# Kernel optimization log

Hardware: AMD Instinct MI355X
Metric: run time of the kernel (lower is better)

Reference implementation:

```python
import jax, jax.numpy as jnp
import numpy as np

EPS = 1e-12

def setup_inputs() -> dict:
    key = jax.random.key(0)
    k1, k2, k3, k4, k5, k6 = jax.random.split(key, 6)
    B, DIM, T = 16, 256, 2048
    K, D = 1024, 64  # num_embeddings, embedding_dim
    N = B * T
    input_data = jax.random.normal(k1, (B, DIM, T), dtype=jnp.float32)
    codebooks = jax.random.normal(k2, (K, D), dtype=jnp.float32)
    W_in = jax.random.normal(k3, (DIM, D), dtype=jnp.float32) / np.sqrt(DIM)
    b_in = jnp.zeros((D,), dtype=jnp.float32)
    W_out = jax.random.normal(k4, (D, DIM), dtype=jnp.float32) / np.sqrt(D)
    b_out = jnp.zeros((DIM,), dtype=jnp.float32)
    random_vector = jax.random.normal(k5, (N, D), dtype=jnp.float32)
    return {"input_data": input_data, "codebooks": codebooks,
            "W_in": W_in, "b_in": b_in, "W_out": W_out, "b_out": b_out,
            "random_vector": random_vector}

def reference(input_data, codebooks, W_in, b_in, W_out, b_out, random_vector):
    B, DIM, T = input_data.shape
    D = codebooks.shape[1]
    # encode: [B, DIM, T] -> [B, T, DIM] -> project -> [B*T, D]
    x = jnp.einsum('bct,cd->btd', input_data, W_in) + b_in
    x = x.reshape(-1, D)  # [N, D]
    distances = (jnp.sum(x * x, axis=1, keepdims=True)
                 - 2.0 * (x @ codebooks.T)
                 + jnp.sum(codebooks * codebooks, axis=1)[None, :])  # [N, K]
    min_indices = jnp.argmin(distances, axis=1)  # [N]
    hard = codebooks[min_indices]  # [N, D]
    # noise substitution
    norm_resid = jnp.sqrt(jnp.sum((x - hard) ** 2, axis=1, keepdims=True))
    norm_rand = jnp.sqrt(jnp.sum(random_vector ** 2, axis=1, keepdims=True))
    vq_error = (norm_resid / (norm_rand + EPS)) * random_vector
    q = x + vq_error  # [N, D]
    # decode: [N, D] -> [B, T, D] -> project_out -> [B, DIM, T]
    q = q.reshape(B, T, D)
    out = jnp.einsum('btd,dc->bct', q, W_out) + b_out[None, :, None]
    return out
```

## Files before the change

### kernel.cpp

```cpp
#include <hip/hip_runtime.h>
#include <hip/hip_bf16.h>

typedef __bf16 bf16x8 __attribute__((ext_vector_type(8)));
typedef unsigned short u16x8 __attribute__((ext_vector_type(8)));
typedef unsigned short u16x4 __attribute__((ext_vector_type(4)));
typedef float f32x4 __attribute__((ext_vector_type(4)));
typedef unsigned short u16;

constexpr int DIMc = 256, Tt = 2048, Kk = 1024, Dd = 64;

#define WS_WINT 0
#define WS_CBX  18432
#define WS_WOX  116736

__device__ __forceinline__ u16 f2b(float f) {
  unsigned u = __float_as_uint(f);
  return (u16)((u + 0x7FFFu + ((u >> 16) & 1u)) >> 16);
}
__device__ __forceinline__ float b2f(u16 v) {
  return __uint_as_float(((unsigned)v) << 16);
}
__device__ __forceinline__ f32x4 mfma16(u16x8 a, u16x8 b, f32x4 c) {
  return __builtin_amdgcn_mfma_f32_16x16x32_bf16(
      __builtin_bit_cast(bf16x8, a), __builtin_bit_cast(bf16x8, b), c, 0, 0, 0);
}
__device__ __forceinline__ void dma16(const u16* g, u16* l) {
  __builtin_amdgcn_global_load_lds(
      (const __attribute__((address_space(1))) unsigned int*)g,
      (__attribute__((address_space(3))) unsigned int*)l, 16, 0, 0);
}

__global__ void nsvq_prep(const float* __restrict__ cb, const float* __restrict__ Win,
                          const float* __restrict__ bin, const float* __restrict__ Wout,
                          const float* __restrict__ bout, u16* __restrict__ wsu) {
  const int g = blockIdx.x * 256 + threadIdx.x;
  u16* WinT = wsu + WS_WINT;
  u16* CbX  = wsu + WS_CBX;
  u16* WoX  = wsu + WS_WOX;
  for (int i = g; i < 16384; i += 8192) {
    int c = i >> 6, d = i & 63;
    WinT[d * 288 + c] = f2b(Win[i]);
  }
  if (g < 2048) {
    int d = g >> 5, j = g & 31; u16 v = 0;
    float bv = bin[d]; u16 h = f2b(bv);
    if (j == 0) v = h; else if (j == 1) v = f2b(bv - b2f(h));
    WinT[d * 288 + 256 + j] = v;
  }
  if (g < 1024) {
    const float4* cr = (const float4*)(cb + (size_t)g * 64);
    float vb[64]; float cn = 0.f;
    #pragma unroll
    for (int q = 0; q < 16; ++q) {
      float4 v = cr[q];
      vb[q*4] = v.x; vb[q*4+1] = v.y; vb[q*4+2] = v.z; vb[q*4+3] = v.w;
      cn = fmaf(v.x, v.x, fmaf(v.y, v.y, fmaf(v.z, v.z, fmaf(v.w, v.w, cn))));
    }
    u16* row = CbX + g * 96;
    #pragma unroll
    for (int d = 0; d < 64; ++d) row[d] = f2b(-2.f * vb[d]);
    u16 h = f2b(cn);
    row[64] = h; row[65] = f2b(cn - b2f(h));
    for (int j = 66; j < 96; ++j) row[j] = 0;
  }
  for (int i = g; i < 16384; i += 8192) {
    int d = i >> 8, c = i & 255;
    WoX[c * 96 + d] = f2b(Wout[i]);
  }
  {
    int c = g >> 5, j = g & 31; u16 v = 0;
    float bv = bout[c]; u16 h = f2b(bv);
    if (j == 0) v = h; else if (j == 1) v = f2b(bv - b2f(h));
    WoX[c * 96 + 64 + j] = v;
  }
}

__global__ __launch_bounds__(512, 2) void nsvq_main(
    const float* __restrict__ in, const float* __restrict__ rnd,
    const u16* __restrict__ wsu, float* __restrict__ out) {
  __shared__ u16 buf[24576];
  __shared__ u16 InT[128 * 256];
  __shared__ u16 Xt[128 * 64];
  __shared__ float mnp[8][128];

  const int tid = threadIdx.x;
  const int lane = tid & 63;
  const int w = tid >> 6;
  const int quad = lane >> 4, col = lane & 15;
  const int b  = blockIdx.x >> 4;
  const int t0 = (blockIdx.x & 15) << 7;
  const int myt = w * 16 + col;

  {
    const int t = tid & 127, cg = tid >> 7;
    const float* ib = in + (size_t)b * DIMc * Tt + t0 + t;
    #pragma unroll
    for (int it = 0; it < 8; ++it) {
      int c0 = cg * 8 + it * 32;
      u16x8 pk;
      #pragma unroll
      for (int j = 0; j < 8; ++j) pk[j] = f2b(ib[(size_t)(c0 + j) * Tt]);
      *(u16x8*)(InT + t * 256 + ((((c0 >> 3)) ^ (t & 7)) << 3)) = pk;
    }
  }
  #pragma unroll
  for (int ii = 0; ii < 5; ++ii) {
    int i = w + 8 * ii;
    if (i < 36) dma16(wsu + WS_WINT + i * 512 + lane * 8, buf + i * 512);
  }
  float rr2v = 0.f;
  const float* rb = rnd + ((size_t)b * Tt + t0) * Dd;
  #pragma unroll
  for (int tt = 0; tt < 16; ++tt) {
    float v = rb[(size_t)(w * 16 + tt) * Dd + lane];
    float s = v * v;
    s += __shfl_xor(s, 1);  s += __shfl_xor(s, 2);  s += __shfl_xor(s, 4);
    s += __shfl_xor(s, 8);  s += __shfl_xor(s, 16); s += __shfl_xor(s, 32);
    if (col == tt) rr2v = s;
  }
  __syncthreads();

  u16x8 Bc1 = {0, 0, 0, 0, 0, 0, 0, 0};
  if (quad == 0) { Bc1[0] = 0x3F80; Bc1[1] = 0x3F80; }
  f32x4 acc[4];
  {
    u16x8 Bf[8];
    #pragma unroll
    for (int kt = 0; kt < 8; ++kt)
      Bf[kt] = *(const u16x8*)(InT + myt * 256 + (((kt * 4 + quad) ^ (myt & 7)) << 3));
    #pragma unroll
    for (int mt = 0; mt < 4; ++mt) {
      f32x4 a = {0.f, 0.f, 0.f, 0.f};
      #pragma unroll
      for (int kt = 0; kt < 8; ++kt) {
        u16x8 A = *(const u16x8*)(buf + (mt * 16 + col) * 288 + kt * 32 + quad * 8);
        a = mfma16(A, Bf[kt], a);
      }
      u16x8 A8 = *(const u16x8*)(buf + (mt * 16 + col) * 288 + 256 + quad * 8);
      acc[mt] = mfma16(A8, Bc1, a);
    }
  }
  float x2v = 0.f;
  #pragma unroll
  for (int mt = 0; mt < 4; ++mt) {
    u16x4 pk;
    #pragma unroll
    for (int r = 0; r < 4; ++r) { x2v = fmaf(acc[mt][r], acc[mt][r], x2v); pk[r] = f2b(acc[mt][r]); }
    int bk = mt * 2 + (quad >> 1);
    *(u16x4*)(Xt + myt * 64 + ((bk ^ (myt & 7)) << 3) + (quad & 1) * 4) = pk;
  }
  x2v += __shfl_xor(x2v, 16);
  x2v += __shfl_xor(x2v, 32);
  __syncthreads();

  u16x8 Xa[8], Xb[8];
  #pragma unroll
  for (int nt = 0; nt < 8; ++nt) {
    int tr = nt * 16 + col;
    Xa[nt] = *(const u16x8*)(Xt + tr * 64 + ((quad ^ (tr & 7)) << 3));
    Xb[nt] = *(const u16x8*)(Xt + tr * 64 + (((4 + quad) ^ (tr & 7)) << 3));
  }
  float minv[8];
  #pragma unroll
  for (int i = 0; i < 8; ++i) minv[i] = 3.4e38f;
  for (int ch = 0; ch < 4; ++ch) {
    if (ch) __syncthreads();
    #pragma unroll
    for (int ii = 0; ii < 6; ++ii) {
      int i = w + 8 * ii;
      dma16(wsu + WS_CBX + ch * 24576 + i * 512 + lane * 8, buf + i * 512);
    }
    __syncthreads();
    #pragma unroll
    for (int ms = 0; ms < 2; ++ms) {
      const u16* ar = buf + (w * 32 + ms * 16 + col) * 96;
      u16x8 A0 = *(const u16x8*)(ar + quad * 8);
      u16x8 A1 = *(const u16x8*)(ar + 32 + quad * 8);
      u16x8 A2 = *(const u16x8*)(ar + 64 + quad * 8);
      #pragma unroll
      for (int nt = 0; nt < 8; ++nt) {
        f32x4 a = {0.f, 0.f, 0.f, 0.f};
        a = mfma16(A0, Xa[nt], a);
        a = mfma16(A1, Xb[nt], a);
        a = mfma16(A2, Bc1, a);
        #pragma unroll
        for (int r = 0; r < 4; ++r) minv[nt] = fminf(minv[nt], a[r]);
      }
    }
  }
  #pragma unroll
  for (int nt = 0; nt < 8; ++nt) {
    float m = minv[nt];
    m = fminf(m, __shfl_xor(m, 16));
    m = fminf(m, __shfl_xor(m, 32));
    mnp[w][nt * 16 + col] = m;
  }
  __syncthreads();

  #pragma unroll
  for (int ii = 0; ii < 6; ++ii) {
    int i = w + 8 * ii;
    dma16(wsu + WS_WOX + i * 512 + lane * 8, buf + i * 512);
  }
  float mv = 3.4e38f;
  #pragma unroll
  for (int j = 0; j < 8; ++j) mv = fminf(mv, mnp[j][myt]);
  float r2  = fmaxf(x2v + mv, 0.f);
  float scv = sqrtf(r2) / (sqrtf(rr2v) + 1e-12f);
  #pragma unroll
  for (int tt = 0; tt < 16; ++tt) {
    float s = __shfl(scv, tt);
    float rv = rb[(size_t)(w * 16 + tt) * Dd + lane];
    int tr = w * 16 + tt;
    int idx = tr * 64 + (((lane >> 3) ^ (tr & 7)) << 3) + (lane & 7);
    Xt[idx] = f2b(fmaf(s, rv, b2f(Xt[idx])));
  }
  __syncthreads();

  u16x8 Q0 = *(const u16x8*)(Xt + myt * 64 + ((quad ^ (myt & 7)) << 3));
  u16x8 Q1 = *(const u16x8*)(Xt + myt * 64 + (((4 + quad) ^ (myt & 7)) << 3));
  float* ob0 = out + (size_t)b * DIMc * Tt + t0 + myt;
  #pragma unroll
  for (int mt = 0; mt < 16; ++mt) {
    const u16* ar = buf + (mt * 16 + col) * 96;
    u16x8 A0 = *(const u16x8*)(ar + quad * 8);
    u16x8 A1 = *(const u16x8*)(ar + 32 + quad * 8);
    u16x8 A2 = *(const u16x8*)(ar + 64 + quad * 8);
    f32x4 a = {0.f, 0.f, 0.f, 0.f};
    a = mfma16(A0, Q0, a);
    a = mfma16(A1, Q1, a);
    a = mfma16(A2, Bc1, a);
    float* ob = ob0 + (size_t)(mt * 16 + quad * 4) * Tt;
    #pragma unroll
    for (int r = 0; r < 4; ++r) ob[(size_t)r * Tt] = a[r];
  }
}

extern "C" void kernel_launch(void* const* d_in, const int* in_sizes, int n_in,
                              void* d_out, int out_size, void* d_ws, size_t ws_size,
                              hipStream_t stream) {
  const float *in = nullptr, *cb = nullptr, *rnd = nullptr, *bin = nullptr, *bout = nullptr;
  const float* w16[2] = {nullptr, nullptr}; int nw = 0;
  for (int i = 0; i < n_in; ++i) {
    switch (in_sizes[i]) {
      case 8388608: in  = (const float*)d_in[i]; break;
      case 65536:   cb  = (const float*)d_in[i]; break;
      case 2097152: rnd = (const float*)d_in[i]; break;
      case 64:      bin = (const float*)d_in[i]; break;
      case 256:     bout= (const float*)d_in[i]; break;
      case 16384:   if (nw < 2) w16[nw++] = (const float*)d_in[i]; break;
      default: break;
    }
  }
  if (!in)  in  = (const float*)d_in[0];
  if (!cb)  cb  = (const float*)d_in[1];
  if (nw < 2) { w16[0] = (const float*)d_in[2]; w16[1] = (const float*)d_in[4]; }
  if (!bin) bin = (const float*)d_in[3];
  if (!bout) bout = (const float*)d_in[5];
  if (!rnd) rnd = (const float*)d_in[6];

  u16* wsu = (u16*)d_ws;
  float* outp = (float*)d_out;

  nsvq_prep<<<32, 256, 0, stream>>>(cb, w16[0], bin, w16[1], bout, wsu);
  nsvq_main<<<256, 512, 0, stream>>>(in, rnd, wsu, outp);
}
```

Before: 116.0 us.

## Halve tile size, double-buffer codebook chunks, fold biases and norms into accumulators

Each block now handles 64 time steps with 256 threads, giving 512 blocks instead of 256 for more parallelism. The codebook is streamed in 8 double-buffered chunks so loads overlap the distance MFMAs. The bias and codebook-norm terms now initialise the fp32 accumulators instead of riding along as extra bf16 hi/lo MFMA columns, which drops one MFMA per tile and shrinks the padded rows. The random vector is loaded once into registers, used for both its norm and the noise update, and the update is fused with the x values still held in registers. The trade-off is that each smaller block reloads the full codebook and weights.

New measurement: 126.5 us. +9.1%, slower.

```diff
diff --git a/kernel.cpp b/kernel.cpp
--- a/kernel.cpp
+++ b/kernel.cpp
@@ -10,15 +10,13 @@
 constexpr int DIMc = 256, Tt = 2048, Kk = 1024, Dd = 64;
 
 #define WS_WINT 0
-#define WS_CBX  18432
-#define WS_WOX  116736
+#define WS_CBX  16896
+#define WS_WOX  90624
+#define WS_CN_F 54528
 
 __device__ __forceinline__ u16 f2b(float f) {
   unsigned u = __float_as_uint(f);
   return (u16)((u + 0x7FFFu + ((u >> 16) & 1u)) >> 16);
-}
-__device__ __forceinline__ float b2f(u16 v) {
-  return __uint_as_float(((unsigned)v) << 16);
 }
 __device__ __forceinline__ f32x4 mfma16(u16x8 a, u16x8 b, f32x4 c) {
   return __builtin_amdgcn_mfma_f32_16x16x32_bf16(
@@ -31,97 +29,68 @@
 }
 
 __global__ void nsvq_prep(const float* __restrict__ cb, const float* __restrict__ Win,
-                          const float* __restrict__ bin, const float* __restrict__ Wout,
-                          const float* __restrict__ bout, u16* __restrict__ wsu) {
+                          const float* __restrict__ Wout, u16* __restrict__ wsu) {
   const int g = blockIdx.x * 256 + threadIdx.x;
-  u16* WinT = wsu + WS_WINT;
-  u16* CbX  = wsu + WS_CBX;
-  u16* WoX  = wsu + WS_WOX;
   for (int i = g; i < 16384; i += 8192) {
     int c = i >> 6, d = i & 63;
-    WinT[d * 288 + c] = f2b(Win[i]);
-  }
-  if (g < 2048) {
-    int d = g >> 5, j = g & 31; u16 v = 0;
-    float bv = bin[d]; u16 h = f2b(bv);
-    if (j == 0) v = h; else if (j == 1) v = f2b(bv - b2f(h));
-    WinT[d * 288 + 256 + j] = v;
+    wsu[WS_WINT + d * 264 + c] = f2b(Win[i]);
+  }
+  for (int i = g; i < 65536; i += 8192) {
+    int k = i >> 6, d = i & 63;
+    wsu[WS_CBX + k * 72 + d] = f2b(-2.f * cb[i]);
+  }
+  for (int i = g; i < 16384; i += 8192) {
+    int d = i >> 8, c = i & 255;
+    wsu[WS_WOX + c * 72 + d] = f2b(Wout[i]);
   }
   if (g < 1024) {
     const float4* cr = (const float4*)(cb + (size_t)g * 64);
-    float vb[64]; float cn = 0.f;
+    float cn = 0.f;
     #pragma unroll
     for (int q = 0; q < 16; ++q) {
       float4 v = cr[q];
-      vb[q*4] = v.x; vb[q*4+1] = v.y; vb[q*4+2] = v.z; vb[q*4+3] = v.w;
       cn = fmaf(v.x, v.x, fmaf(v.y, v.y, fmaf(v.z, v.z, fmaf(v.w, v.w, cn))));
     }
-    u16* row = CbX + g * 96;
-    #pragma unroll
-    for (int d = 0; d < 64; ++d) row[d] = f2b(-2.f * vb[d]);
-    u16 h = f2b(cn);
-    row[64] = h; row[65] = f2b(cn - b2f(h));
-    for (int j = 66; j < 96; ++j) row[j] = 0;
-  }
-  for (int i = g; i < 16384; i += 8192) {
-    int d = i >> 8, c = i & 255;
-    WoX[c * 96 + d] = f2b(Wout[i]);
-  }
+    ((float*)wsu)[WS_CN_F + g] = cn;
+  }
+}
+
+__global__ __launch_bounds__(256, 2) void nsvq_main(
+    const float* __restrict__ in, const float* __restrict__ rnd,
+    const float* __restrict__ bin, const float* __restrict__ bout,
+    const u16* __restrict__ wsu, const float* __restrict__ cnorm,
+    float* __restrict__ out) {
+  __shared__ u16 buf[18432];
+  __shared__ u16 InT[64 * 256];
+  __shared__ u16 Xt[64 * 64];
+  __shared__ float mnp[4][64];
+
+  const int tid  = threadIdx.x;
+  const int lane = tid & 63;
+  const int w    = tid >> 6;
+  const int quad = lane >> 4, col = lane & 15;
+  const int b  = blockIdx.x >> 5;
+  const int t0 = (blockIdx.x & 31) << 6;
+  const int myt = w * 16 + col;
+
   {
-    int c = g >> 5, j = g & 31; u16 v = 0;
-    float bv = bout[c]; u16 h = f2b(bv);
-    if (j == 0) v = h; else if (j == 1) v = f2b(bv - b2f(h));
-    WoX[c * 96 + 64 + j] = v;
-  }
-}
-
-__global__ __launch_bounds__(512, 2) void nsvq_main(
-    const float* __restrict__ in, const float* __restrict__ rnd,
-    const u16* __restrict__ wsu, float* __restrict__ out) {
-  __shared__ u16 buf[24576];
-  __shared__ u16 InT[128 * 256];
-  __shared__ u16 Xt[128 * 64];
-  __shared__ float mnp[8][128];
-
-  const int tid = threadIdx.x;
-  const int lane = tid & 63;
-  const int w = tid >> 6;
-  const int quad = lane >> 4, col = lane & 15;
-  const int b  = blockIdx.x >> 4;
-  const int t0 = (blockIdx.x & 15) << 7;
-  const int myt = w * 16 + col;
-
-  {
-    const int t = tid & 127, cg = tid >> 7;
-    const float* ib = in + (size_t)b * DIMc * Tt + t0 + t;
+    const float* ib = in + (size_t)b * DIMc * Tt + t0 + lane;
     #pragma unroll
     for (int it = 0; it < 8; ++it) {
-      int c0 = cg * 8 + it * 32;
+      int c0 = w * 64 + it * 8;
       u16x8 pk;
       #pragma unroll
       for (int j = 0; j < 8; ++j) pk[j] = f2b(ib[(size_t)(c0 + j) * Tt]);
-      *(u16x8*)(InT + t * 256 + ((((c0 >> 3)) ^ (t & 7)) << 3)) = pk;
-    }
-  }
-  #pragma unroll
-  for (int ii = 0; ii < 5; ++ii) {
-    int i = w + 8 * ii;
-    if (i < 36) dma16(wsu + WS_WINT + i * 512 + lane * 8, buf + i * 512);
-  }
-  float rr2v = 0.f;
-  const float* rb = rnd + ((size_t)b * Tt + t0) * Dd;
-  #pragma unroll
-  for (int tt = 0; tt < 16; ++tt) {
-    float v = rb[(size_t)(w * 16 + tt) * Dd + lane];
-    float s = v * v;
-    s += __shfl_xor(s, 1);  s += __shfl_xor(s, 2);  s += __shfl_xor(s, 4);
-    s += __shfl_xor(s, 8);  s += __shfl_xor(s, 16); s += __shfl_xor(s, 32);
-    if (col == tt) rr2v = s;
-  }
-  __syncthreads();
-
-  u16x8 Bc1 = {0, 0, 0, 0, 0, 0, 0, 0};
-  if (quad == 0) { Bc1[0] = 0x3F80; Bc1[1] = 0x3F80; }
+      *(u16x8*)(InT + lane * 256 + (((c0 >> 3) ^ (lane & 7)) << 3)) = pk;
+    }
+  }
+  #pragma unroll
+  for (int ii = 0; ii < 9; ++ii) {
+    int i = w + 4 * ii;
+    if (i < 33) dma16(wsu + WS_WINT + i * 512 + lane * 8, buf + i * 512);
+  }
+  __syncthreads();
+
   f32x4 acc[4];
   {
     u16x8 Bf[8];
@@ -130,14 +99,12 @@
       Bf[kt] = *(const u16x8*)(InT + myt * 256 + (((kt * 4 + quad) ^ (myt & 7)) << 3));
     #pragma unroll
     for (int mt = 0; mt < 4; ++mt) {
-      f32x4 a = {0.f, 0.f, 0.f, 0.f};
+      acc[mt] = *(const f32x4*)(bin + mt * 16 + quad * 4);
       #pragma unroll
       for (int kt = 0; kt < 8; ++kt) {
-        u16x8 A = *(const u16x8*)(buf + (mt * 16 + col) * 288 + kt * 32 + quad * 8);
-        a = mfma16(A, Bf[kt], a);
+        u16x8 A = *(const u16x8*)(buf + (mt * 16 + col) * 264 + kt * 32 + quad * 8);
+        acc[mt] = mfma16(A, Bf[kt], acc[mt]);
       }
-      u16x8 A8 = *(const u16x8*)(buf + (mt * 16 + col) * 288 + 256 + quad * 8);
-      acc[mt] = mfma16(A8, Bc1, a);
     }
   }
   float x2v = 0.f;
@@ -153,43 +120,56 @@
   x2v += __shfl_xor(x2v, 32);
   __syncthreads();
 
-  u16x8 Xa[8], Xb[8];
-  #pragma unroll
-  for (int nt = 0; nt < 8; ++nt) {
+  const float* rp = rnd + ((size_t)(b * Tt) + t0 + myt) * Dd;
+  f32x4 rv[4];
+  #pragma unroll
+  for (int mt = 0; mt < 4; ++mt) rv[mt] = *(const f32x4*)(rp + mt * 16 + quad * 4);
+
+  u16x8 Xa[4], Xb[4];
+  #pragma unroll
+  for (int nt = 0; nt < 4; ++nt) {
     int tr = nt * 16 + col;
     Xa[nt] = *(const u16x8*)(Xt + tr * 64 + ((quad ^ (tr & 7)) << 3));
     Xb[nt] = *(const u16x8*)(Xt + tr * 64 + (((4 + quad) ^ (tr & 7)) << 3));
   }
-  float minv[8];
-  #pragma unroll
-  for (int i = 0; i < 8; ++i) minv[i] = 3.4e38f;
-  for (int ch = 0; ch < 4; ++ch) {
-    if (ch) __syncthreads();
-    #pragma unroll
-    for (int ii = 0; ii < 6; ++ii) {
-      int i = w + 8 * ii;
-      dma16(wsu + WS_CBX + ch * 24576 + i * 512 + lane * 8, buf + i * 512);
-    }
-    __syncthreads();
-    #pragma unroll
-    for (int ms = 0; ms < 2; ++ms) {
-      const u16* ar = buf + (w * 32 + ms * 16 + col) * 96;
-      u16x8 A0 = *(const u16x8*)(ar + quad * 8);
-      u16x8 A1 = *(const u16x8*)(ar + 32 + quad * 8);
-      u16x8 A2 = *(const u16x8*)(ar + 64 + quad * 8);
+  float minv[4] = {3.4e38f, 3.4e38f, 3.4e38f, 3.4e38f};
+  {
+    #pragma unroll
+    for (int ii = 0; ii < 5; ++ii) {
+      int i = w + 4 * ii;
+      if (i < 18) dma16(wsu + WS_CBX + i * 512 + lane * 8, buf + i * 512);
+    }
+    for (int ch = 0; ch < 8; ++ch) {
+      __syncthreads();
+      if (ch < 7) {
+        const u16* src = wsu + WS_CBX + (ch + 1) * 9216;
+        u16* dst = buf + ((ch + 1) & 1) * 9216;
+        #pragma unroll
+        for (int ii = 0; ii < 5; ++ii) {
+          int i = w + 4 * ii;
+          if (i < 18) dma16(src + i * 512 + lane * 8, dst + i * 512);
+        }
+      }
+      const u16* cbase = buf + (ch & 1) * 9216;
       #pragma unroll
-      for (int nt = 0; nt < 8; ++nt) {
-        f32x4 a = {0.f, 0.f, 0.f, 0.f};
-        a = mfma16(A0, Xa[nt], a);
-        a = mfma16(A1, Xb[nt], a);
-        a = mfma16(A2, Bc1, a);
+      for (int ms = 0; ms < 2; ++ms) {
+        f32x4 cn = *(const f32x4*)(cnorm + ch * 128 + w * 32 + ms * 16 + quad * 4);
+        const u16* ar = cbase + (w * 32 + ms * 16 + col) * 72;
+        u16x8 A0 = *(const u16x8*)(ar + quad * 8);
+        u16x8 A1 = *(const u16x8*)(ar + 32 + quad * 8);
         #pragma unroll
-        for (int r = 0; r < 4; ++r) minv[nt] = fminf(minv[nt], a[r]);
+        for (int nt = 0; nt < 4; ++nt) {
+          f32x4 a = cn;
+          a = mfma16(A0, Xa[nt], a);
+          a = mfma16(A1, Xb[nt], a);
+          #pragma unroll
+          for (int r = 0; r < 4; ++r) minv[nt] = fminf(minv[nt], a[r]);
+        }
       }
     }
   }
   #pragma unroll
-  for (int nt = 0; nt < 8; ++nt) {
+  for (int nt = 0; nt < 4; ++nt) {
     float m = minv[nt];
     m = fminf(m, __shfl_xor(m, 16));
     m = fminf(m, __shfl_xor(m, 32));
@@ -198,22 +178,27 @@
   __syncthreads();
 
   #pragma unroll
-  for (int ii = 0; ii < 6; ++ii) {
-    int i = w + 8 * ii;
+  for (int ii = 0; ii < 9; ++ii) {
+    int i = w + 4 * ii;
     dma16(wsu + WS_WOX + i * 512 + lane * 8, buf + i * 512);
   }
-  float mv = 3.4e38f;
-  #pragma unroll
-  for (int j = 0; j < 8; ++j) mv = fminf(mv, mnp[j][myt]);
+  float rr2v = 0.f;
+  #pragma unroll
+  for (int mt = 0; mt < 4; ++mt)
+    #pragma unroll
+    for (int r = 0; r < 4; ++r) rr2v = fmaf(rv[mt][r], rv[mt][r], rr2v);
+  rr2v += __shfl_xor(rr2v, 16);
+  rr2v += __shfl_xor(rr2v, 32);
+  float mv = fminf(fminf(mnp[0][myt], mnp[1][myt]), fminf(mnp[2][myt], mnp[3][myt]));
   float r2  = fmaxf(x2v + mv, 0.f);
   float scv = sqrtf(r2) / (sqrtf(rr2v) + 1e-12f);
   #pragma unroll
-  for (int tt = 0; tt < 16; ++tt) {
-    float s = __shfl(scv, tt);
-    float rv = rb[(size_t)(w * 16 + tt) * Dd + lane];
-    int tr = w * 16 + tt;
-    int idx = tr * 64 + (((lane >> 3) ^ (tr & 7)) << 3) + (lane & 7);
-    Xt[idx] = f2b(fmaf(s, rv, b2f(Xt[idx])));
+  for (int mt = 0; mt < 4; ++mt) {
+    u16x4 pk;
+    #pragma unroll
+    for (int r = 0; r < 4; ++r) pk[r] = f2b(fmaf(scv, rv[mt][r], acc[mt][r]));
+    int bk = mt * 2 + (quad >> 1);
+    *(u16x4*)(Xt + myt * 64 + ((bk ^ (myt & 7)) << 3) + (quad & 1) * 4) = pk;
   }
   __syncthreads();
 
@@ -222,17 +207,14 @@
   float* ob0 = out + (size_t)b * DIMc * Tt + t0 + myt;
   #pragma unroll
   for (int mt = 0; mt < 16; ++mt) {
-    const u16* ar = buf + (mt * 16 + col) * 96;
+    f32x4 a = *(const f32x4*)(bout + mt * 16 + quad * 4);
+    const u16* ar = buf + (mt * 16 + col) * 72;
     u16x8 A0 = *(const u16x8*)(ar + quad * 8);
     u16x8 A1 = *(const u16x8*)(ar + 32 + quad * 8);
-    u16x8 A2 = *(const u16x8*)(ar + 64 + quad * 8);
-    f32x4 a = {0.f, 0.f, 0.f, 0.f};
     a = mfma16(A0, Q0, a);
     a = mfma16(A1, Q1, a);
-    a = mfma16(A2, Bc1, a);
-    float* ob = ob0 + (size_t)(mt * 16 + quad * 4) * Tt;
-    #pragma unroll
-    for (int r = 0; r < 4; ++r) ob[(size_t)r * Tt] = a[r];
+    #pragma unroll
+    for (int r = 0; r < 4; ++r) ob0[(size_t)(mt * 16 + quad * 4 + r) * Tt] = a[r];
   }
 }
 
@@ -260,8 +242,9 @@
   if (!rnd) rnd = (const float*)d_in[6];
 
   u16* wsu = (u16*)d_ws;
+  const float* cnorm = (const float*)d_ws + WS_CN_F;
   float* outp = (float*)d_out;
 
-  nsvq_prep<<<32, 256, 0, stream>>>(cb, w16[0], bin, w16[1], bout, wsu);
-  nsvq_main<<<256, 512, 0, stream>>>(in, rnd, wsu, outp);
-}
+  nsvq_prep<<<32, 256, 0, stream>>>(cb, w16[0], w16[1], wsu);
+  nsvq_main<<<512, 256, 0, stream>>>(in, rnd, bin, bout, wsu, cnorm, outp);
+}
```
